# Kernel tuning notes

Hardware: AMD Instinct MI355X
Metric: run time of the kernel (lower is better)

## Reference

```python
import jax, jax.numpy as jnp
import numpy as np

UNITS = 256
INNER_ITERS = 1
INNER_LR = [0.01]
LN_EPS = 1e-3  # keras LayerNormalization default epsilon
B, L, F = 512, 128, 128


def _encoder(W1, b1, W2, b2, z):
    # keras 'gelu' activation is exact (approximate=False)
    h = jax.nn.gelu(z @ W1 + b1, approximate=False)
    return h @ W2 + b2


def _layer_norm(z, g, b):
    m = jnp.mean(z, axis=-1, keepdims=True)
    v = jnp.var(z, axis=-1, keepdims=True)
    return g * (z - m) / jnp.sqrt(v + LN_EPS) + b


def setup_inputs():
    U = UNITS
    key = jax.random.key(0)
    ks = jax.random.split(key, 12)
    s = 0.02
    return {
        "inputs": jax.random.normal(ks[0], (B, F), jnp.float32),
        "prev_hidden": jax.random.normal(ks[1], (B, U), jnp.float32),
        "sequence_buffer": jax.random.normal(ks[2], (B, L, U), jnp.float32),
        "Wp": jax.random.normal(ks[3], (F, U)) * s, "bp": jnp.zeros((U,)),
        "Wphi": jax.random.normal(ks[4], (U, U)) * s, "bphi": jnp.zeros((U,)),
        "Wpsi": jax.random.normal(ks[5], (U, U)) * s, "bpsi": jnp.zeros((U,)),
        "W1": jax.random.normal(ks[6], (U, 4 * U)) * s, "b1": jnp.zeros((4 * U,)),
        "W2": jax.random.normal(ks[7], (4 * U, U)) * s, "b2": jnp.zeros((U,)),
        "Wg": jax.random.normal(ks[8], (U, U)) * s, "g_bias": jnp.zeros((U,)),
        "ln_g": jnp.ones((U,)), "ln_b": jnp.zeros((U,)),
        "Wh": jax.random.normal(ks[9], (U, U)) * s, "h_bias": jnp.zeros((U,)),
    }


def reference(inputs, prev_hidden, sequence_buffer, Wp, bp, Wphi, bphi, Wpsi, bpsi,
              W1, b1, W2, b2, Wg, g_bias, ln_g, ln_b, Wh, h_bias):
    U = UNITS
    bsz = inputs.shape[0]
    # input projection (F != units)
    proj = inputs @ Wp + bp                                   # [B, U]
    # shift buffer, append projected input
    buf = jnp.concatenate([sequence_buffer[:, 1:, :], proj[:, None, :]], axis=1)  # [B, L, U]
    x = buf[:, :-1, :].reshape(-1, U)                         # [B*(L-1), U]
    y = buf[:, 1:, :].reshape(-1, U)
    phi = x @ Wphi + bphi

    params = (W1, b1, W2, b2)

    def inner_loss(p):
        rec = _layer_norm(_encoder(*p, phi) @ Wg + g_bias, ln_g, ln_b)
        return jnp.mean(jnp.square(rec - y)), rec

    rec = None
    for it in range(INNER_ITERS):
        (_, rec), grads = jax.value_and_grad(inner_loss, has_aux=True)(params)
        lr = INNER_LR[min(it, len(INNER_LR) - 1)]
        params = tuple(p - lr * g for p, g in zip(params, grads))

    psi = buf[:, -1, :] @ Wpsi + bpsi                         # [B, U]
    contrib = jnp.mean(rec.reshape(bsz, -1, U), axis=1)       # [B, U]
    # psi path uses the UPDATED inner-encoder weights
    out = (_encoder(*params, psi) + contrib) @ Wh + h_bias    # [B, U]
    return out, buf
```

## Files before the change

### kernel.cpp

```cpp
#include <hip/hip_runtime.h>
#include <cmath>

typedef __bf16 bf16;
typedef __attribute__((ext_vector_type(8))) __bf16 bf16x8;
typedef __attribute__((ext_vector_type(4))) float f32x4;
typedef __attribute__((ext_vector_type(2))) unsigned int u32x2;

constexpr int NROWS = 512 * 127;
constexpr float LR = 0.01f;
constexpr float INV_NU = 1.f / (65024.f * 256.f);

__device__ __forceinline__ float geluf(float x) {
  return 0.5f * x * (1.f + erff(x * 0.70710678118654752f));
}
__device__ __forceinline__ float dgeluf(float x) {
  float c = 0.5f * (1.f + erff(x * 0.70710678118654752f));
  float p = 0.3989422804014327f * __expf(-0.5f * x * x);
  return c + x * p;
}
__device__ __forceinline__ bf16x8 gelu8(bf16x8 v) {
  bf16x8 o;
#pragma unroll
  for (int i = 0; i < 8; i++) o[i] = (bf16)geluf((float)v[i]);
  return o;
}
__device__ __forceinline__ bf16x8 gelu8f(bf16x8 v) {
  bf16x8 o;
#pragma unroll
  for (int i = 0; i < 8; i++) {
    float x = (float)v[i];
    o[i] = (bf16)(x / (1.f + __expf(-1.702f * x)));
  }
  return o;
}

template <int EPI, bool GA>
__global__ __launch_bounds__(256) void gemm_k(
    const bf16* __restrict__ A, const bf16* __restrict__ Bt,
    const float* __restrict__ bias, void* __restrict__ out0,
    void* __restrict__ out1, const bf16* __restrict__ aux,
    int M, int N, int K) {
  __shared__ bf16 As[128][40];
  __shared__ bf16 Bs[128][40];
  const int t = threadIdx.x;
  const int bm = blockIdx.x * 128, bn = blockIdx.y * 128;
  const int lane = t & 63, w = t >> 6;
  const int wr = w >> 1, wc = w & 1;

  f32x4 acc[4][4];
#pragma unroll
  for (int mi = 0; mi < 4; mi++)
#pragma unroll
    for (int ni = 0; ni < 4; ni++) {
      f32x4 z = {0.f, 0.f, 0.f, 0.f};
      acc[mi][ni] = z;
    }

  const int r2 = t >> 2;
  const int c8 = (t & 3) * 8;

  for (int kt = 0; kt < K; kt += 32) {
    __syncthreads();
    {
      bf16x8 a0 = *(const bf16x8*)(A + (size_t)(bm + r2) * K + kt + c8);
      bf16x8 a1 = *(const bf16x8*)(A + (size_t)(bm + r2 + 64) * K + kt + c8);
      bf16x8 b0 = *(const bf16x8*)(Bt + (size_t)(bn + r2) * K + kt + c8);
      bf16x8 b1 = *(const bf16x8*)(Bt + (size_t)(bn + r2 + 64) * K + kt + c8);
      if constexpr (GA) { a0 = gelu8(a0); a1 = gelu8(a1); }
      *(bf16x8*)&As[r2][c8] = a0;
      *(bf16x8*)&As[r2 + 64][c8] = a1;
      *(bf16x8*)&Bs[r2][c8] = b0;
      *(bf16x8*)&Bs[r2 + 64][c8] = b1;
    }
    __syncthreads();
    bf16x8 af[4], bfr[4];
#pragma unroll
    for (int mi = 0; mi < 4; mi++)
      af[mi] = *(const bf16x8*)&As[wr * 64 + mi * 16 + (lane & 15)][(lane >> 4) * 8];
#pragma unroll
    for (int ni = 0; ni < 4; ni++)
      bfr[ni] = *(const bf16x8*)&Bs[wc * 64 + ni * 16 + (lane & 15)][(lane >> 4) * 8];
#pragma unroll
    for (int mi = 0; mi < 4; mi++)
#pragma unroll
      for (int ni = 0; ni < 4; ni++)
        acc[mi][ni] = __builtin_amdgcn_mfma_f32_16x16x32_bf16(af[mi], bfr[ni], acc[mi][ni], 0, 0, 0);
  }

#pragma unroll
  for (int ni = 0; ni < 4; ni++) {
    const int col = bn + wc * 64 + ni * 16 + (lane & 15);
    const float bv = bias ? bias[col] : 0.f;
#pragma unroll
    for (int mi = 0; mi < 4; mi++) {
      const int rb = bm + wr * 64 + mi * 16 + ((lane >> 4) << 2);
#pragma unroll
      for (int r = 0; r < 4; r++) {
        float v = acc[mi][ni][r] + bv;
        size_t idx = (size_t)(rb + r) * N + col;
        if constexpr (EPI == 0) {
          ((float*)out0)[idx] = v;
        } else if constexpr (EPI == 1) {
          ((bf16*)out0)[idx] = (bf16)v;
        } else if constexpr (EPI == 2) {
          ((bf16*)out0)[idx] = (bf16)v;
          ((bf16*)out1)[idx] = (bf16)geluf(v);
        } else if constexpr (EPI == 3) {
          ((bf16*)out0)[idx] = (bf16)geluf(v);
        } else {
          float a = (float)aux[idx];
          ((bf16*)out0)[idx] = (bf16)(v * dgeluf(a));
        }
      }
    }
  }
}

template <bool GELU_A>
__global__ __launch_bounds__(256) void tgemm3_k(
    const bf16* __restrict__ Asrc, const bf16* __restrict__ Bsrc,
    float* __restrict__ outP, int M, int N, int ldA, int ldB, int K) {
  __shared__ __align__(16) bf16 As[4736];
  __shared__ __align__(16) bf16 Bs[4736];
  const int t = threadIdx.x;
  const int bm = blockIdx.x * 128, bn = blockIdx.y * 128;
  const int r0 = blockIdx.z * 1024;
  const int rows = (K - r0 < 1024) ? (K - r0) : 1024;
  const int lane = t & 63, w = t >> 6, wr = w >> 1, wc = w & 1;

  f32x4 acc[4][4];
#pragma unroll
  for (int mi = 0; mi < 4; mi++)
#pragma unroll
    for (int ni = 0; ni < 4; ni++) {
      f32x4 z = {0.f, 0.f, 0.f, 0.f};
      acc[mi][ni] = z;
    }

  const bool isB = t >= 128;
  const int srow = (t & 127) >> 4;
  const int scol = (t & 15) * 8;
  const int sms = (t & 15) >> 1;
  const int shalf = (t & 1) * 8;
  const bf16* src = isB ? Bsrc : Asrc;
  const int ld = isB ? ldB : ldA;
  const int bx = isB ? bn : bm;
  bf16* dst = isB ? Bs : As;

  const unsigned abase = (unsigned)(size_t)(void*)As;
  const unsigned bbase = (unsigned)(size_t)(void*)Bs;
  const int g = lane >> 4;
  const int ml = lane & 15;
  const unsigned acol0 = abase + 2u * (unsigned)((wr * 4) * 592 + g * 144 + ml);
  const unsigned bcol0 = bbase + 2u * (unsigned)((wc * 4) * 592 + g * 144 + ml);

  for (int kt = 0; kt < rows; kt += 32) {
    __syncthreads();
#pragma unroll
    for (int ll = 0; ll < 4; ll++) {
      const int row = srow + ll * 8;
      bf16x8 v = *(const bf16x8*)(src + (size_t)(r0 + kt + row) * ld + bx + scol);
      if constexpr (GELU_A) { if (!isB) v = gelu8f(v); }
      *(bf16x8*)&dst[sms * 592 + ll * 144 + srow * 16 + shalf] = v;
    }
    __syncthreads();

    union FR { u32x2 p[2]; bf16x8 v; };
    FR af[4], bfr[4];
#pragma unroll
    for (int mi = 0; mi < 4; mi++) {
      const unsigned a = acol0 + (unsigned)(mi * 592 * 2);
      asm volatile("ds_read_b64_tr_b16 %0, %1" : "=v"(af[mi].p[0]) : "v"(a));
      asm volatile("ds_read_b64_tr_b16 %0, %1 offset:128" : "=v"(af[mi].p[1]) : "v"(a));
    }
#pragma unroll
    for (int ni = 0; ni < 4; ni++) {
      const unsigned b = bcol0 + (unsigned)(ni * 592 * 2);
      asm volatile("ds_read_b64_tr_b16 %0, %1" : "=v"(bfr[ni].p[0]) : "v"(b));
      asm volatile("ds_read_b64_tr_b16 %0, %1 offset:128" : "=v"(bfr[ni].p[1]) : "v"(b));
    }
    asm volatile("s_waitcnt lgkmcnt(0)" ::: "memory");
    __builtin_amdgcn_sched_barrier(0);

#pragma unroll
    for (int mi = 0; mi < 4; mi++)
#pragma unroll
      for (int ni = 0; ni < 4; ni++)
        acc[mi][ni] = __builtin_amdgcn_mfma_f32_16x16x32_bf16(af[mi].v, bfr[ni].v, acc[mi][ni], 0, 0, 0);
  }

  float* o = outP + (size_t)blockIdx.z * M * N;
#pragma unroll
  for (int ni = 0; ni < 4; ni++) {
    const int col = bn + wc * 64 + ni * 16 + (lane & 15);
#pragma unroll
    for (int mi = 0; mi < 4; mi++) {
      const int rb = bm + wr * 64 + mi * 16 + ((lane >> 4) << 2);
#pragma unroll
      for (int r = 0; r < 4; r++) o[(size_t)(rb + r) * N + col] = acc[mi][ni][r];
    }
  }
}

__global__ void prep_k(const float* inputs, const float* Wp, const float* Wphi,
                       const float* W1, const float* W2, const float* Wg,
                       const float* Wpsi, const float* Wh,
                       bf16* inb, bf16* WpT, bf16* WphiT, bf16* W1T, bf16* W2T,
                       bf16* WgT, bf16* Wgb, bf16* W2b, bf16* WpsiT, bf16* WhT) {
  int i = blockIdx.x * 256 + threadIdx.x;
  if (i < 65536) {
    inb[i] = (bf16)inputs[i];
  } else if ((i -= 65536) < 32768) {
    int u = i >> 7, f = i & 127;
    WpT[i] = (bf16)Wp[f * 256 + u];
  } else if ((i -= 32768) < 65536) {
    int n = i >> 8, k = i & 255;
    WphiT[i] = (bf16)Wphi[k * 256 + n];
  } else if ((i -= 65536) < 262144) {
    int h = i >> 8, u = i & 255;
    W1T[i] = (bf16)W1[u * 1024 + h];
  } else if ((i -= 262144) < 262144) {
    int u = i >> 10, h = i & 1023;
    W2T[i] = (bf16)W2[h * 256 + u];
  } else if ((i -= 262144) < 65536) {
    int n = i >> 8, k = i & 255;
    WgT[i] = (bf16)Wg[k * 256 + n];
  } else if ((i -= 65536) < 65536) {
    Wgb[i] = (bf16)Wg[i];
  } else if ((i -= 65536) < 262144) {
    W2b[i] = (bf16)W2[i];
  } else if ((i -= 262144) < 65536) {
    int n = i >> 8, k = i & 255;
    WpsiT[i] = (bf16)Wpsi[k * 256 + n];
  } else if ((i -= 65536) < 65536) {
    int n = i >> 8, k = i & 255;
    WhT[i] = (bf16)Wh[k * 256 + n];
  }
}

__global__ void xcast_k(const float* __restrict__ seq, bf16* __restrict__ xb) {
  int v8 = blockIdx.x * 256 + threadIdx.x;
  int r = v8 >> 5, c8 = (v8 & 31) * 8;
  int b = r / 127, t = r - b * 127;
  const float* src = seq + ((size_t)(b * 128 + t + 1)) * 256 + c8;
  float4 v0 = *(const float4*)(src);
  float4 v1 = *(const float4*)(src + 4);
  bf16x8 o;
  o[0] = (bf16)v0.x; o[1] = (bf16)v0.y; o[2] = (bf16)v0.z; o[3] = (bf16)v0.w;
  o[4] = (bf16)v1.x; o[5] = (bf16)v1.y; o[6] = (bf16)v1.z; o[7] = (bf16)v1.w;
  *(bf16x8*)(xb + (size_t)r * 256 + c8) = o;
}

__global__ void projcast_k(const float* __restrict__ proj, bf16* __restrict__ projb) {
  int i = blockIdx.x * 256 + threadIdx.x;
  projb[i] = (bf16)proj[i];
}

__global__ void bufwrite_k(const float* __restrict__ seq, const float* __restrict__ proj,
                           float* __restrict__ buf) {
  int i = blockIdx.x * 256 + threadIdx.x;
  int b = i >> 13, rem = i & 8191;
  int j = rem >> 6, c4 = (rem & 63) * 4;
  float4 v;
  if (j < 127)
    v = *(const float4*)(seq + ((size_t)(b * 128 + j + 1)) * 256 + c4);
  else
    v = *(const float4*)(proj + (size_t)b * 256 + c4);
  *(float4*)(buf + ((size_t)(b * 128 + j)) * 256 + c4) = v;
}

__global__ __launch_bounds__(256) void ln_k(const bf16* zin, bf16* dzout,
                                            const float* __restrict__ seq,
                                            const float* __restrict__ proj,
                                            const float* __restrict__ lng,
                                            const float* __restrict__ lnb,
                                            bf16* __restrict__ rec) {
  const int w = threadIdx.x >> 6, lane = threadIdx.x & 63;
  const int r = blockIdx.x * 4 + w;
  const int b = r / 127, tt = r - b * 127;
  typedef __attribute__((ext_vector_type(4))) __bf16 bf16x4;
  bf16x4 zv = *(const bf16x4*)(zin + (size_t)r * 256 + lane * 4);
  float z0 = (float)zv[0], z1 = (float)zv[1], z2 = (float)zv[2], z3 = (float)zv[3];
  float s1 = z0 + z1 + z2 + z3;
  float s2 = z0 * z0 + z1 * z1 + z2 * z2 + z3 * z3;
  for (int m = 1; m < 64; m <<= 1) { s1 += __shfl_xor(s1, m); s2 += __shfl_xor(s2, m); }
  const float mean = s1 * (1.f / 256.f);
  const float var = s2 * (1.f / 256.f) - mean * mean;
  const float rs = rsqrtf(var + 1e-3f);
  const float4 gv = *(const float4*)(lng + lane * 4);
  const float4 bv = *(const float4*)(lnb + lane * 4);
  const float* ysrc = (tt < 126) ? (seq + ((size_t)(b * 128 + tt + 2)) * 256)
                                 : (proj + (size_t)b * 256);
  const float4 yv = *(const float4*)(ysrc + lane * 4);
  float xh0 = (z0 - mean) * rs, xh1 = (z1 - mean) * rs, xh2 = (z2 - mean) * rs, xh3 = (z3 - mean) * rs;
  float r0 = gv.x * xh0 + bv.x, r1 = gv.y * xh1 + bv.y, r2 = gv.z * xh2 + bv.z, r3 = gv.w * xh3 + bv.w;
  float u0 = 2.f * (r0 - yv.x) * INV_NU * gv.x;
  float u1 = 2.f * (r1 - yv.y) * INV_NU * gv.y;
  float u2 = 2.f * (r2 - yv.z) * INV_NU * gv.z;
  float u3 = 2.f * (r3 - yv.w) * INV_NU * gv.w;
  float t1 = u0 + u1 + u2 + u3;
  float t2 = u0 * xh0 + u1 * xh1 + u2 * xh2 + u3 * xh3;
  for (int m = 1; m < 64; m <<= 1) { t1 += __shfl_xor(t1, m); t2 += __shfl_xor(t2, m); }
  const float mu = t1 * (1.f / 256.f), mux = t2 * (1.f / 256.f);
  bf16x4 ro, dzo;
  ro[0] = (bf16)r0; ro[1] = (bf16)r1; ro[2] = (bf16)r2; ro[3] = (bf16)r3;
  dzo[0] = (bf16)((u0 - mu - xh0 * mux) * rs);
  dzo[1] = (bf16)((u1 - mu - xh1 * mux) * rs);
  dzo[2] = (bf16)((u2 - mu - xh2 * mux) * rs);
  dzo[3] = (bf16)((u3 - mu - xh3 * mux) * rs);
  *(bf16x4*)(rec + (size_t)r * 256 + lane * 4) = ro;
  *(bf16x4*)(dzout + (size_t)r * 256 + lane * 4) = dzo;
}

__global__ void colsum_k(const bf16* __restrict__ src, float* __restrict__ part, int C) {
  const int col = blockIdx.x * 256 + threadIdx.x;
  const int ch = blockIdx.y;
  float s = 0.f;
  const int rbeg = ch * 1016;
  for (int rr = rbeg; rr < rbeg + 1016; rr++) s += (float)src[(size_t)rr * C + col];
  part[(size_t)ch * C + col] = s;
}

__global__ void contrib_k(const bf16* __restrict__ rec, float* __restrict__ contrib) {
  const int b = blockIdx.x, u = threadIdx.x;
  float s = 0.f;
  for (int t = 0; t < 127; t++) s += (float)rec[((size_t)b * 127 + t) * 256 + u];
  contrib[b * 256 + u] = s * (1.f / 127.f);
}

__global__ void update2_k(const float* __restrict__ pW2, const float* __restrict__ pdb2,
                          const float* __restrict__ W2, const float* __restrict__ b2,
                          bf16* __restrict__ W2pT, float* __restrict__ b2p) {
  int idx = blockIdx.x * 256 + threadIdx.x;
  if (idx < 262144) {
    float s = 0.f;
    for (int z = 0; z < 64; z++) s += pW2[(size_t)z * 262144 + idx];
    int h = idx >> 8, u = idx & 255;
    W2pT[(size_t)u * 1024 + h] = (bf16)(W2[idx] - LR * s);
  } else {
    int u = idx - 262144;
    float s = 0.f;
    for (int c = 0; c < 64; c++) s += pdb2[c * 256 + u];
    b2p[u] = b2[u] - LR * s;
  }
}

__global__ void update1_k(const float* __restrict__ pW1, const float* __restrict__ pdb1,
                          const float* __restrict__ W1, const float* __restrict__ b1,
                          bf16* __restrict__ W1pT, float* __restrict__ b1p) {
  int idx = blockIdx.x * 256 + threadIdx.x;
  if (idx < 262144) {
    float s = 0.f;
    for (int z = 0; z < 64; z++) s += pW1[(size_t)z * 262144 + idx];
    int u = idx >> 10, h = idx & 1023;
    W1pT[(size_t)h * 256 + u] = (bf16)(W1[idx] - LR * s);
  } else {
    int h = idx - 262144;
    float s = 0.f;
    for (int c = 0; c < 64; c++) s += pdb1[c * 1024 + h];
    b1p[h] = b1[h] - LR * s;
  }
}

__global__ void fin_k(const float* __restrict__ encp, const float* __restrict__ contrib,
                      bf16* __restrict__ fin) {
  int i = blockIdx.x * 256 + threadIdx.x;
  fin[i] = (bf16)(encp[i] + contrib[i]);
}

extern "C" void kernel_launch(void* const* d_in, const int* in_sizes, int n_in,
                              void* d_out, int out_size, void* d_ws, size_t ws_size,
                              hipStream_t stream) {
  const float* inputs = (const float*)d_in[0];
  const float* seq = (const float*)d_in[2];
  const float* Wp = (const float*)d_in[3];
  const float* bp = (const float*)d_in[4];
  const float* Wphi = (const float*)d_in[5];
  const float* bphi = (const float*)d_in[6];
  const float* Wpsi = (const float*)d_in[7];
  const float* bpsi = (const float*)d_in[8];
  const float* W1 = (const float*)d_in[9];
  const float* b1 = (const float*)d_in[10];
  const float* W2 = (const float*)d_in[11];
  const float* b2 = (const float*)d_in[12];
  const float* Wg = (const float*)d_in[13];
  const float* gbias = (const float*)d_in[14];
  const float* lng = (const float*)d_in[15];
  const float* lnb = (const float*)d_in[16];
  const float* Wh = (const float*)d_in[17];
  const float* hbias = (const float*)d_in[18];

  float* out = (float*)d_out;
  float* buf = out + 131072;
  float* pW2 = buf;
  float* pW1 = buf;

  char* wptr = (char*)d_ws;
  auto alloc = [&](size_t bytes) {
    char* p = wptr;
    wptr += (bytes + 255) & ~(size_t)255;
    return p;
  };
  bf16* inb   = (bf16*)alloc(65536 * 2);
  bf16* WpT   = (bf16*)alloc(32768 * 2);
  bf16* WphiT = (bf16*)alloc(65536 * 2);
  bf16* W1T   = (bf16*)alloc(262144 * 2);
  bf16* W2T   = (bf16*)alloc(262144 * 2);
  bf16* WgT   = (bf16*)alloc(65536 * 2);
  bf16* Wgb   = (bf16*)alloc(65536 * 2);
  bf16* W2b   = (bf16*)alloc(262144 * 2);
  bf16* WpsiT = (bf16*)alloc(65536 * 2);
  bf16* WhT   = (bf16*)alloc(65536 * 2);
  bf16* W1pT  = (bf16*)alloc(262144 * 2);
  bf16* W2pT  = (bf16*)alloc(262144 * 2);
  float* b1p  = (float*)alloc(1024 * 4);
  float* b2p  = (float*)alloc(256 * 4);
  float* proj = (float*)alloc(131072 * 4);
  bf16* projb = (bf16*)alloc(131072 * 2);
  float* pdb2 = (float*)alloc(64 * 256 * 4);
  float* pdb1 = (float*)alloc(64 * 1024 * 4);
  bf16* psib  = (bf16*)alloc(131072 * 2);
  bf16* hpb   = (bf16*)alloc(524288 * 2);
  float* encp = (float*)alloc(131072 * 4);
  float* contrib = (float*)alloc(131072 * 4);
  bf16* finb  = (bf16*)alloc(131072 * 2);
  const size_t NU = (size_t)NROWS * 256;
  const size_t NH = (size_t)NROWS * 1024;
  bf16* xz     = (bf16*)alloc(NU * 2);
  bf16* phi    = (bf16*)alloc(NU * 2);
  bf16* a1b    = (bf16*)alloc(NH * 2);
  bf16* encden = (bf16*)alloc(NU * 2);
  const bool useH = ws_size >= (size_t)((char*)wptr - (char*)d_ws) + NH * 2 + 4096;
  bf16* hbuf = useH ? (bf16*)alloc(NH * 2) : nullptr;

  prep_k<<<4736, 256, 0, stream>>>(inputs, Wp, Wphi, W1, W2, Wg, Wpsi, Wh,
                                   inb, WpT, WphiT, W1T, W2T, WgT, Wgb, W2b, WpsiT, WhT);
  xcast_k<<<8128, 256, 0, stream>>>(seq, xz);
  gemm_k<0, false><<<dim3(4, 2), 256, 0, stream>>>(inb, WpT, bp, proj, nullptr, nullptr, 512, 256, 128);
  projcast_k<<<512, 256, 0, stream>>>(proj, projb);
  gemm_k<1, false><<<dim3(508, 2), 256, 0, stream>>>(xz, WphiT, bphi, phi, nullptr, nullptr, NROWS, 256, 256);
  if (useH)
    gemm_k<2, false><<<dim3(508, 8), 256, 0, stream>>>(phi, W1T, b1, a1b, hbuf, nullptr, NROWS, 1024, 256);
  else
    gemm_k<1, false><<<dim3(508, 8), 256, 0, stream>>>(phi, W1T, b1, a1b, nullptr, nullptr, NROWS, 1024, 256);
  if (useH)
    gemm_k<1, false><<<dim3(508, 2), 256, 0, stream>>>(hbuf, W2T, b2, encden, nullptr, nullptr, NROWS, 256, 1024);
  else
    gemm_k<1, true><<<dim3(508, 2), 256, 0, stream>>>(a1b, W2T, b2, encden, nullptr, nullptr, NROWS, 256, 1024);
  gemm_k<1, false><<<dim3(508, 2), 256, 0, stream>>>(encden, WgT, gbias, xz, nullptr, nullptr, NROWS, 256, 256);
  ln_k<<<16256, 256, 0, stream>>>(xz, xz, seq, proj, lng, lnb, encden);
  contrib_k<<<512, 256, 0, stream>>>(encden, contrib);
  gemm_k<1, false><<<dim3(508, 2), 256, 0, stream>>>(xz, Wgb, nullptr, encden, nullptr, nullptr, NROWS, 256, 256);
  colsum_k<<<dim3(1, 64), 256, 0, stream>>>(encden, pdb2, 256);
  if (useH)
    tgemm3_k<false><<<dim3(8, 2, 64), 256, 0, stream>>>(hbuf, encden, pW2, 1024, 256, 1024, 256, NROWS);
  else
    tgemm3_k<true><<<dim3(8, 2, 64), 256, 0, stream>>>(a1b, encden, pW2, 1024, 256, 1024, 256, NROWS);
  update2_k<<<1025, 256, 0, stream>>>(pW2, pdb2, W2, b2, W2pT, b2p);
  gemm_k<5, false><<<dim3(508, 8), 256, 0, stream>>>(encden, W2b, nullptr, a1b, nullptr, a1b, NROWS, 1024, 256);
  colsum_k<<<dim3(4, 64), 256, 0, stream>>>(a1b, pdb1, 1024);
  tgemm3_k<false><<<dim3(2, 8, 64), 256, 0, stream>>>(phi, a1b, pW1, 256, 1024, 256, 1024, NROWS);
  update1_k<<<1028, 256, 0, stream>>>(pW1, pdb1, W1, b1, W1pT, b1p);
  bufwrite_k<<<16384, 256, 0, stream>>>(seq, proj, buf);
  gemm_k<1, false><<<dim3(4, 2), 256, 0, stream>>>(projb, WpsiT, bpsi, psib, nullptr, nullptr, 512, 256, 256);
  gemm_k<3, false><<<dim3(4, 8), 256, 0, stream>>>(psib, W1pT, b1p, hpb, nullptr, nullptr, 512, 1024, 256);
  gemm_k<0, false><<<dim3(4, 2), 256, 0, stream>>>(hpb, W2pT, b2p, encp, nullptr, nullptr, 512, 256, 1024);
  fin_k<<<512, 256, 0, stream>>>(encp, contrib, finb);
  gemm_k<0, false><<<dim3(4, 2), 256, 0, stream>>>(finb, WhT, hbias, out, nullptr, nullptr, 512, 256, 256);
}
```

Measured before the change: 1.074 ms.

## Add GEMM kernel with direct global-to-LDS loads, swizzled LDS, K=64 tiles

Adds gemm2_k, which uses global_load_lds to copy tiles straight from global memory into XOR-swizzled shared memory and steps K by 64 instead of 32. This halves the number of barriers per K and avoids round-tripping the tile data through registers. The grid is transposed so N-tiles vary fastest, letting consecutive blocks share A rows in cache. All non-GELU-A GEMM launches switch to it, and the old kernel is kept only for the fallback path. Loads are still not double-buffered, so global latency stays exposed between the two barriers.

After: 1.023 ms. -4.7%, faster.

```diff
diff --git a/kernel.cpp b/kernel.cpp
--- a/kernel.cpp
+++ b/kernel.cpp
@@ -34,16 +34,23 @@
   return o;
 }
 
-template <int EPI, bool GA>
-__global__ __launch_bounds__(256) void gemm_k(
+__device__ __forceinline__ void gload16(const bf16* g, const bf16* lds) {
+  __builtin_amdgcn_global_load_lds(
+      (const __attribute__((address_space(1))) unsigned int*)(size_t)(const void*)g,
+      (__attribute__((address_space(3))) unsigned int*)(unsigned)(size_t)(const void*)lds,
+      16, 0, 0);
+}
+
+template <int EPI>
+__global__ __launch_bounds__(256) void gemm2_k(
     const bf16* __restrict__ A, const bf16* __restrict__ Bt,
     const float* __restrict__ bias, void* __restrict__ out0,
     void* __restrict__ out1, const bf16* __restrict__ aux,
     int M, int N, int K) {
-  __shared__ bf16 As[128][40];
-  __shared__ bf16 Bs[128][40];
+  __shared__ __align__(16) bf16 As[128 * 64];
+  __shared__ __align__(16) bf16 Bs[128 * 64];
   const int t = threadIdx.x;
-  const int bm = blockIdx.x * 128, bn = blockIdx.y * 128;
+  const int bn = blockIdx.x * 128, bm = blockIdx.y * 128;
   const int lane = t & 63, w = t >> 6;
   const int wr = w >> 1, wc = w & 1;
 
@@ -56,35 +63,49 @@
       acc[mi][ni] = z;
     }
 
-  const int r2 = t >> 2;
-  const int c8 = (t & 3) * 8;
-
-  for (int kt = 0; kt < K; kt += 32) {
+  const int l8 = lane >> 3;
+  const int p = lane & 7;
+  const int csw = p ^ l8;
+  const bf16* aS[4];
+  const bf16* bS[4];
+#pragma unroll
+  for (int i = 0; i < 4; i++) {
+    const int r = 32 * w + 8 * i + l8;
+    aS[i] = A + (size_t)(bm + r) * K + csw * 8;
+    bS[i] = Bt + (size_t)(bn + r) * K + csw * 8;
+  }
+
+  const int ml = lane & 15, g = lane >> 4;
+  const int c0 = g ^ (ml & 7);
+  const int c1 = (4 | g) ^ (ml & 7);
+
+  for (int kt = 0; kt < K; kt += 64) {
     __syncthreads();
-    {
-      bf16x8 a0 = *(const bf16x8*)(A + (size_t)(bm + r2) * K + kt + c8);
-      bf16x8 a1 = *(const bf16x8*)(A + (size_t)(bm + r2 + 64) * K + kt + c8);
-      bf16x8 b0 = *(const bf16x8*)(Bt + (size_t)(bn + r2) * K + kt + c8);
-      bf16x8 b1 = *(const bf16x8*)(Bt + (size_t)(bn + r2 + 64) * K + kt + c8);
-      if constexpr (GA) { a0 = gelu8(a0); a1 = gelu8(a1); }
-      *(bf16x8*)&As[r2][c8] = a0;
-      *(bf16x8*)&As[r2 + 64][c8] = a1;
-      *(bf16x8*)&Bs[r2][c8] = b0;
-      *(bf16x8*)&Bs[r2 + 64][c8] = b1;
+#pragma unroll
+    for (int i = 0; i < 4; i++) {
+      gload16(aS[i], As + (32 * w + 8 * i) * 64);
+      gload16(bS[i], Bs + (32 * w + 8 * i) * 64);
+      aS[i] += 64; bS[i] += 64;
     }
     __syncthreads();
-    bf16x8 af[4], bfr[4];
-#pragma unroll
-    for (int mi = 0; mi < 4; mi++)
-      af[mi] = *(const bf16x8*)&As[wr * 64 + mi * 16 + (lane & 15)][(lane >> 4) * 8];
-#pragma unroll
-    for (int ni = 0; ni < 4; ni++)
-      bfr[ni] = *(const bf16x8*)&Bs[wc * 64 + ni * 16 + (lane & 15)][(lane >> 4) * 8];
-#pragma unroll
-    for (int mi = 0; mi < 4; mi++)
-#pragma unroll
-      for (int ni = 0; ni < 4; ni++)
-        acc[mi][ni] = __builtin_amdgcn_mfma_f32_16x16x32_bf16(af[mi], bfr[ni], acc[mi][ni], 0, 0, 0);
+
+    bf16x8 af[2][4], bfr[2][4];
+#pragma unroll
+    for (int mi = 0; mi < 4; mi++) {
+      const int m = wr * 64 + mi * 16 + ml;
+      const int n = wc * 64 + mi * 16 + ml;
+      af[0][mi] = *(const bf16x8*)&As[m * 64 + c0 * 8];
+      af[1][mi] = *(const bf16x8*)&As[m * 64 + c1 * 8];
+      bfr[0][mi] = *(const bf16x8*)&Bs[n * 64 + c0 * 8];
+      bfr[1][mi] = *(const bf16x8*)&Bs[n * 64 + c1 * 8];
+    }
+#pragma unroll
+    for (int ks = 0; ks < 2; ks++)
+#pragma unroll
+      for (int mi = 0; mi < 4; mi++)
+#pragma unroll
+        for (int ni = 0; ni < 4; ni++)
+          acc[mi][ni] = __builtin_amdgcn_mfma_f32_16x16x32_bf16(af[ks][mi], bfr[ks][ni], acc[mi][ni], 0, 0, 0);
   }
 
 #pragma unroll
@@ -110,6 +131,79 @@
         } else {
           float a = (float)aux[idx];
           ((bf16*)out0)[idx] = (bf16)(v * dgeluf(a));
+        }
+      }
+    }
+  }
+}
+
+template <int EPI, bool GA>
+__global__ __launch_bounds__(256) void gemm_k(
+    const bf16* __restrict__ A, const bf16* __restrict__ Bt,
+    const float* __restrict__ bias, void* __restrict__ out0,
+    void* __restrict__ out1, const bf16* __restrict__ aux,
+    int M, int N, int K) {
+  __shared__ bf16 As[128][40];
+  __shared__ bf16 Bs[128][40];
+  const int t = threadIdx.x;
+  const int bm = blockIdx.x * 128, bn = blockIdx.y * 128;
+  const int lane = t & 63, w = t >> 6;
+  const int wr = w >> 1, wc = w & 1;
+
+  f32x4 acc[4][4];
+#pragma unroll
+  for (int mi = 0; mi < 4; mi++)
+#pragma unroll
+    for (int ni = 0; ni < 4; ni++) {
+      f32x4 z = {0.f, 0.f, 0.f, 0.f};
+      acc[mi][ni] = z;
+    }
+  const int r2 = t >> 2;
+  const int c8 = (t & 3) * 8;
+
+  for (int kt = 0; kt < K; kt += 32) {
+    __syncthreads();
+    {
+      bf16x8 a0 = *(const bf16x8*)(A + (size_t)(bm + r2) * K + kt + c8);
+      bf16x8 a1 = *(const bf16x8*)(A + (size_t)(bm + r2 + 64) * K + kt + c8);
+      bf16x8 b0 = *(const bf16x8*)(Bt + (size_t)(bn + r2) * K + kt + c8);
+      bf16x8 b1 = *(const bf16x8*)(Bt + (size_t)(bn + r2 + 64) * K + kt + c8);
+      if constexpr (GA) { a0 = gelu8(a0); a1 = gelu8(a1); }
+      *(bf16x8*)&As[r2][c8] = a0;
+      *(bf16x8*)&As[r2 + 64][c8] = a1;
+      *(bf16x8*)&Bs[r2][c8] = b0;
+      *(bf16x8*)&Bs[r2 + 64][c8] = b1;
+    }
+    __syncthreads();
+    bf16x8 af[4], bfr[4];
+#pragma unroll
+    for (int mi = 0; mi < 4; mi++)
+      af[mi] = *(const bf16x8*)&As[wr * 64 + mi * 16 + (lane & 15)][(lane >> 4) * 8];
+#pragma unroll
+    for (int ni = 0; ni < 4; ni++)
+      bfr[ni] = *(const bf16x8*)&Bs[wc * 64 + ni * 16 + (lane & 15)][(lane >> 4) * 8];
+#pragma unroll
+    for (int mi = 0; mi < 4; mi++)
+#pragma unroll
+      for (int ni = 0; ni < 4; ni++)
+        acc[mi][ni] = __builtin_amdgcn_mfma_f32_16x16x32_bf16(af[mi], bfr[ni], acc[mi][ni], 0, 0, 0);
+  }
+
+#pragma unroll
+  for (int ni = 0; ni < 4; ni++) {
+    const int col = bn + wc * 64 + ni * 16 + (lane & 15);
+    const float bv = bias ? bias[col] : 0.f;
+#pragma unroll
+    for (int mi = 0; mi < 4; mi++) {
+      const int rb = bm + wr * 64 + mi * 16 + ((lane >> 4) << 2);
+#pragma unroll
+      for (int r = 0; r < 4; r++) {
+        float v = acc[mi][ni][r] + bv;
+        size_t idx = (size_t)(rb + r) * N + col;
+        if constexpr (EPI == 1) {
+          ((bf16*)out0)[idx] = (bf16)v;
+        } else {
+          ((float*)out0)[idx] = v;
         }
       }
     }
@@ -436,35 +530,35 @@
   prep_k<<<4736, 256, 0, stream>>>(inputs, Wp, Wphi, W1, W2, Wg, Wpsi, Wh,
                                    inb, WpT, WphiT, W1T, W2T, WgT, Wgb, W2b, WpsiT, WhT);
   xcast_k<<<8128, 256, 0, stream>>>(seq, xz);
-  gemm_k<0, false><<<dim3(4, 2), 256, 0, stream>>>(inb, WpT, bp, proj, nullptr, nullptr, 512, 256, 128);
+  gemm2_k<0><<<dim3(2, 4), 256, 0, stream>>>(inb, WpT, bp, proj, nullptr, nullptr, 512, 256, 128);
   projcast_k<<<512, 256, 0, stream>>>(proj, projb);
-  gemm_k<1, false><<<dim3(508, 2), 256, 0, stream>>>(xz, WphiT, bphi, phi, nullptr, nullptr, NROWS, 256, 256);
+  gemm2_k<1><<<dim3(2, 508), 256, 0, stream>>>(xz, WphiT, bphi, phi, nullptr, nullptr, NROWS, 256, 256);
   if (useH)
-    gemm_k<2, false><<<dim3(508, 8), 256, 0, stream>>>(phi, W1T, b1, a1b, hbuf, nullptr, NROWS, 1024, 256);
+    gemm2_k<2><<<dim3(8, 508), 256, 0, stream>>>(phi, W1T, b1, a1b, hbuf, nullptr, NROWS, 1024, 256);
   else
-    gemm_k<1, false><<<dim3(508, 8), 256, 0, stream>>>(phi, W1T, b1, a1b, nullptr, nullptr, NROWS, 1024, 256);
+    gemm2_k<1><<<dim3(8, 508), 256, 0, stream>>>(phi, W1T, b1, a1b, nullptr, nullptr, NROWS, 1024, 256);
   if (useH)
-    gemm_k<1, false><<<dim3(508, 2), 256, 0, stream>>>(hbuf, W2T, b2, encden, nullptr, nullptr, NROWS, 256, 1024);
+    gemm2_k<1><<<dim3(2, 508), 256, 0, stream>>>(hbuf, W2T, b2, encden, nullptr, nullptr, NROWS, 256, 1024);
   else
     gemm_k<1, true><<<dim3(508, 2), 256, 0, stream>>>(a1b, W2T, b2, encden, nullptr, nullptr, NROWS, 256, 1024);
-  gemm_k<1, false><<<dim3(508, 2), 256, 0, stream>>>(encden, WgT, gbias, xz, nullptr, nullptr, NROWS, 256, 256);
+  gemm2_k<1><<<dim3(2, 508), 256, 0, stream>>>(encden, WgT, gbias, xz, nullptr, nullptr, NROWS, 256, 256);
   ln_k<<<16256, 256, 0, stream>>>(xz, xz, seq, proj, lng, lnb, encden);
   contrib_k<<<512, 256, 0, stream>>>(encden, contrib);
-  gemm_k<1, false><<<dim3(508, 2), 256, 0, stream>>>(xz, Wgb, nullptr, encden, nullptr, nullptr, NROWS, 256, 256);
+  gemm2_k<1><<<dim3(2, 508), 256, 0, stream>>>(xz, Wgb, nullptr, encden, nullptr, nullptr, NROWS, 256, 256);
   colsum_k<<<dim3(1, 64), 256, 0, stream>>>(encden, pdb2, 256);
   if (useH)
     tgemm3_k<false><<<dim3(8, 2, 64), 256, 0, stream>>>(hbuf, encden, pW2, 1024, 256, 1024, 256, NROWS);
   else
     tgemm3_k<true><<<dim3(8, 2, 64), 256, 0, stream>>>(a1b, encden, pW2, 1024, 256, 1024, 256, NROWS);
   update2_k<<<1025, 256, 0, stream>>>(pW2, pdb2, W2, b2, W2pT, b2p);
-  gemm_k<5, false><<<dim3(508, 8), 256, 0, stream>>>(encden, W2b, nullptr, a1b, nullptr, a1b, NROWS, 1024, 256);
+  gemm2_k<5><<<dim3(8, 508), 256, 0, stream>>>(encden, W2b, nullptr, a1b, nullptr, a1b, NROWS, 1024, 256);
   colsum_k<<<dim3(4, 64), 256, 0, stream>>>(a1b, pdb1, 1024);
   tgemm3_k<false><<<dim3(2, 8, 64), 256, 0, stream>>>(phi, a1b, pW1, 256, 1024, 256, 1024, NROWS);
   update1_k<<<1028, 256, 0, stream>>>(pW1, pdb1, W1, b1, W1pT, b1p);
   bufwrite_k<<<16384, 256, 0, stream>>>(seq, proj, buf);
-  gemm_k<1, false><<<dim3(4, 2), 256, 0, stream>>>(projb, WpsiT, bpsi, psib, nullptr, nullptr, 512, 256, 256);
-  gemm_k<3, false><<<dim3(4, 8), 256, 0, stream>>>(psib, W1pT, b1p, hpb, nullptr, nullptr, 512, 1024, 256);
-  gemm_k<0, false><<<dim3(4, 2), 256, 0, stream>>>(hpb, W2pT, b2p, encp, nullptr, nullptr, 512, 256, 1024);
+  gemm2_k<1><<<dim3(2, 4), 256, 0, stream>>>(projb, WpsiT, bpsi, psib, nullptr, nullptr, 512, 256, 256);
+  gemm2_k<3><<<dim3(8, 4), 256, 0, stream>>>(psib, W1pT, b1p, hpb, nullptr, nullptr, 512, 1024, 256);
+  gemm2_k<0><<<dim3(2, 4), 256, 0, stream>>>(hpb, W2pT, b2p, encp, nullptr, nullptr, 512, 256, 1024);
   fin_k<<<512, 256, 0, stream>>>(encp, contrib, finb);
-  gemm_k<0, false><<<dim3(4, 2), 256, 0, stream>>>(finb, WhT, hbias, out, nullptr, nullptr, 512, 256, 256);
-}
+  gemm2_k<0><<<dim3(2, 4), 256, 0, stream>>>(finb, WhT, hbias, out, nullptr, nullptr, 512, 256, 256);
+}
```
